# Kernel optimization log

Measured on AMD Instinct MI355X. Metric: run time of the kernel, lower is better.

Reference implementation:

```python
import jax, jax.numpy as jnp
import numpy as np

B, N, DIN, DOUT, DA = 8, 2048, 128, 128, 2
NEG_SLOPE = 0.2


def setup_inputs() -> dict:
    key = jax.random.key(0)
    k = jax.random.split(key, 7)
    x = jax.random.normal(k[0], (B, N, DIN), dtype=jnp.float32)
    mask = jax.random.randint(k[1], (B, N, N), 0, 2, dtype=jnp.int32)
    s = 1.0 / np.sqrt(DIN)
    Wr = jax.random.uniform(k[2], (DA, DIN), jnp.float32, -s, s)      # linear_row.weight
    Wc = jax.random.uniform(k[3], (DA, DIN), jnp.float32, -s, s)      # linear_col.weight
    sa = 1.0 / np.sqrt(2 * DA)
    Wcat = jax.random.uniform(k[4], (2 * DA,), jnp.float32, -sa, sa)  # linear_concat.weight [1, 2*DA] flattened
    Wx = jax.random.uniform(k[5], (DOUT, DIN), jnp.float32, -s, s)    # linear_x.weight
    bx = jax.random.uniform(k[6], (DOUT,), jnp.float32, -s, s)        # linear_x.bias
    return {"x": x, "mask": mask, "Wr": Wr, "Wc": Wc, "Wcat": Wcat, "Wx": Wx, "bx": bx}


def reference(x, mask, Wr, Wc, Wcat, Wx, bx):
    # Row/col projections to tiny attention dim: [B, N, DA]
    row = jnp.einsum('bnd,ad->bna', x, Wr)
    col = jnp.einsum('bnd,ad->bna', x, Wc)
    # Concat scoring: e_ij = linear_concat(LeakyReLU(cat(row_i, col_j)))
    # decomposes as a1 . LR(row_i) + a2 . LR(col_j) -- avoids materializing [B,N,N,2*DA]
    a1, a2 = Wcat[:DA], Wcat[DA:]
    lr_row = jax.nn.leaky_relu(row, NEG_SLOPE) @ a1   # [B, N]
    lr_col = jax.nn.leaky_relu(col, NEG_SLOPE) @ a2   # [B, N]
    e = lr_row[:, :, None] + lr_col[:, None, :]       # [B, N, N]
    # Masked softmax over columns j
    e = jnp.where(mask > 0, e, jnp.float32(-1e9))
    atten = jax.nn.softmax(e, axis=-1)                # [B, N, N]
    # Value projection + combine
    xv = jnp.einsum('bnd,od->bno', x, Wx) + bx        # [B, N, DOUT]
    out = jnp.einsum('bij,bjo->bio', atten, xv)       # [B, N, DOUT]
    return out
```

## Files before the change

### kernel.cpp

```cpp
#include <hip/hip_runtime.h>


typedef __bf16 bf16x8 __attribute__((ext_vector_type(8)));
typedef __bf16 bf16x4 __attribute__((ext_vector_type(4)));
typedef float  f32x4  __attribute__((ext_vector_type(4)));
typedef int    i32x4  __attribute__((ext_vector_type(4)));

#define MFMA_BF16(a, b, c) __builtin_amdgcn_mfma_f32_16x16x32_bf16((a), (b), (c), 0, 0, 0)

static __device__ __forceinline__ bf16x8 cvt8(f32x4 a, f32x4 b) {
  bf16x8 r;
  r[0] = (__bf16)a[0]; r[1] = (__bf16)a[1]; r[2] = (__bf16)a[2]; r[3] = (__bf16)a[3];
  r[4] = (__bf16)b[0]; r[5] = (__bf16)b[1]; r[6] = (__bf16)b[2]; r[7] = (__bf16)b[3];
  return r;
}

__global__ __launch_bounds__(256) void prep_kernel(
    const float* __restrict__ x, const float* __restrict__ Wc,
    const float* __restrict__ Wcat, const float* __restrict__ Wx,
    const float* __restrict__ bx, __bf16* __restrict__ u,
    __bf16* __restrict__ wcol)
{
  __shared__ __bf16 lds[8192];
  const int blk = blockIdx.x;
  const int b = blk >> 5, mt = blk & 31;
  const int wv = threadIdx.x >> 6, lane = threadIdx.x & 63;
  const int np = lane & 15, G = lane >> 4;
  const int r0 = mt * 64 + wv * 16;

  const float* xp = x + ((size_t)(b * 2048 + r0 + np)) * 128 + G * 8;
  bf16x8 af[4];
#pragma unroll
  for (int kk = 0; kk < 4; ++kk) {
    f32x4 x0 = *(const f32x4*)(xp + kk * 32);
    f32x4 x1 = *(const f32x4*)(xp + kk * 32 + 4);
    af[kk] = cvt8(x0, x1);
  }

  f32x4 acc[8], accC;
#pragma unroll
  for (int n = 0; n < 8; ++n) { acc[n][0] = 0.f; acc[n][1] = 0.f; acc[n][2] = 0.f; acc[n][3] = 0.f; }
  accC[0] = accC[1] = accC[2] = accC[3] = 0.f;

#pragma unroll
  for (int n = 0; n < 8; ++n) {
    const float* wp = Wx + (n * 16 + np) * 128 + G * 8;
#pragma unroll
    for (int kk = 0; kk < 4; ++kk) {
      f32x4 w0 = *(const f32x4*)(wp + kk * 32);
      f32x4 w1 = *(const f32x4*)(wp + kk * 32 + 4);
      acc[n] = MFMA_BF16(af[kk], cvt8(w0, w1), acc[n]);
    }
  }
#pragma unroll
  for (int kk = 0; kk < 4; ++kk) {
    bf16x8 bf;
    if (np < 2) {
      const float* cp = Wc + np * 128 + kk * 32 + G * 8;
      f32x4 c0 = *(const f32x4*)cp;
      f32x4 c1 = *(const f32x4*)(cp + 4);
      bf = cvt8(c0, c1);
    } else {
#pragma unroll
      for (int j = 0; j < 8; ++j) bf[j] = (__bf16)0.0f;
    }
    accC = MFMA_BF16(af[kk], bf, accC);
  }

  const float a20 = Wcat[2], a21 = Wcat[3];
  float wexp[4];
#pragma unroll
  for (int r = 0; r < 4; ++r) {
    float c0 = __shfl(accC[r], lane & 48);
    float c1 = __shfl(accC[r], (lane & 48) | 1);
    c0 = c0 > 0.f ? c0 : 0.2f * c0;
    c1 = c1 > 0.f ? c1 : 0.2f * c1;
    wexp[r] = __expf(c0 * a20 + c1 * a21);
  }
  if (np == 0) {
    bf16x4 w4;
#pragma unroll
    for (int r = 0; r < 4; ++r) w4[r] = (__bf16)wexp[r];
    *(bf16x4*)(wcol + (size_t)b * 2048 + r0 + 4 * G) = w4;
  }

  const int t_rel = wv >> 1;
  const int g_store = (wv & 1) * 2 + (G >> 1);
  const int j0 = (G & 1) * 4;
#pragma unroll
  for (int n = 0; n < 8; ++n) {
    float bxv = bx[n * 16 + np];
    bf16x4 v;
#pragma unroll
    for (int r = 0; r < 4; ++r) v[r] = (__bf16)(wexp[r] * (acc[n][r] + bxv));
    *(bf16x4*)(&lds[(t_rel * 8 + n) * 512 + g_store * 128 + np * 8 + j0]) = v;
  }
  __syncthreads();
  __bf16* dst = u + ((size_t)(b * 64 + mt * 2)) * 4096;
#pragma unroll
  for (int it = 0; it < 4; ++it) {
    int s = it * 256 + threadIdx.x;
    ((i32x4*)dst)[s] = ((const i32x4*)lds)[s];
  }
}

__global__ __launch_bounds__(256) void attn_kernel(
    const int* __restrict__ mask, const __bf16* __restrict__ u,
    const __bf16* __restrict__ wcol, float* __restrict__ out)
{
  const int b = blockIdx.x & 7, mt = blockIdx.x >> 3;
  const int wv = threadIdx.x >> 6, lane = threadIdx.x & 63;
  const int np = lane & 15, G = lane >> 4;
  const int row0 = mt * 64 + wv * 16;
  const long long N = 2048;

  const int* mp = mask + ((size_t)b * N + row0 + np) * N + G * 8;
  const __bf16* up = u + (size_t)b * 64 * 4096 + lane * 8;
  const __bf16* wp = wcol + (size_t)b * 2048 + G * 8;

  f32x4 acc[9];
#pragma unroll
  for (int n = 0; n < 9; ++n) { acc[n][0] = 0.f; acc[n][1] = 0.f; acc[n][2] = 0.f; acc[n][3] = 0.f; }

  i32x4 m0A, m1A, m0B, m1B;
  bf16x8 ufA[8], ufB[8], wfA, wfB;

#define LOADS(t, m0, m1, uf, wf)                                         \
  do {                                                                   \
    const int* mpt = mp + (t) * 32;                                      \
    m0 = *(const i32x4*)mpt;                                             \
    m1 = *(const i32x4*)(mpt + 4);                                       \
    const __bf16* upt = up + (t) * 4096;                                 \
    _Pragma("unroll")                                                    \
    for (int n = 0; n < 8; ++n) uf[n] = *(const bf16x8*)(upt + n * 512); \
    wf = *(const bf16x8*)(wp + (t) * 32);                                \
  } while (0)

#define COMPS(m0, m1, uf, wf)                                            \
  do {                                                                   \
    const __bf16 ONE = (__bf16)1.0f, ZER = (__bf16)0.0f;                 \
    bf16x8 af;                                                           \
    af[0] = m0[0] ? ONE : ZER; af[1] = m0[1] ? ONE : ZER;                \
    af[2] = m0[2] ? ONE : ZER; af[3] = m0[3] ? ONE : ZER;                \
    af[4] = m1[0] ? ONE : ZER; af[5] = m1[1] ? ONE : ZER;                \
    af[6] = m1[2] ? ONE : ZER; af[7] = m1[3] ? ONE : ZER;                \
    bf16x8 wfrag;                                                        \
    _Pragma("unroll")                                                    \
    for (int j = 0; j < 8; ++j) wfrag[j] = (np == 0) ? wf[j] : ZER;      \
    _Pragma("unroll")                                                    \
    for (int n = 0; n < 8; ++n) acc[n] = MFMA_BF16(af, uf[n], acc[n]);   \
    acc[8] = MFMA_BF16(af, wfrag, acc[8]);                               \
  } while (0)

  LOADS(0, m0A, m1A, ufA, wfA);
  LOADS(1, m0B, m1B, ufB, wfB);
  for (int t = 0; t < 64; t += 2) {
    COMPS(m0A, m1A, ufA, wfA);
    if (t + 2 < 64) LOADS(t + 2, m0A, m1A, ufA, wfA);
    COMPS(m0B, m1B, ufB, wfB);
    if (t + 3 < 64) LOADS(t + 3, m0B, m1B, ufB, wfB);
  }
#undef LOADS
#undef COMPS

#pragma unroll
  for (int r = 0; r < 4; ++r) {
    float den = __shfl(acc[8][r], lane & 48);
    float inv = 1.0f / den;
    float* op = out + ((size_t)b * N + row0 + 4 * G + r) * 128 + np;
#pragma unroll
    for (int n = 0; n < 8; ++n) op[n * 16] = acc[n][r] * inv;
  }
}

extern "C" void kernel_launch(void* const* d_in, const int* in_sizes, int n_in,
                              void* d_out, int out_size, void* d_ws, size_t ws_size,
                              hipStream_t stream) {
  const float* x    = (const float*)d_in[0];
  const int*   mask = (const int*)d_in[1];
  const float* Wc   = (const float*)d_in[3];
  const float* Wcat = (const float*)d_in[4];
  const float* Wx   = (const float*)d_in[5];
  const float* bx   = (const float*)d_in[6];
  float* out = (float*)d_out;

  const size_t U_BYTES = (size_t)8 * 64 * 4096 * 2;
  if (ws_size < U_BYTES + 8 * 2048 * 2) return;
  __bf16* u    = (__bf16*)d_ws;
  __bf16* wcol = (__bf16*)((char*)d_ws + U_BYTES);

  prep_kernel<<<256, 256, 0, stream>>>(x, Wc, Wcat, Wx, bx, u, wcol);
  attn_kernel<<<256, 256, 0, stream>>>(mask, u, wcol, out);
}
```

Baseline: 237.9 us.

## Split attention K-dimension across waves with LDS reduction, quadruple grid size

Each attention block now handles 16 rows instead of 64, and its four waves split the 2048-column reduction into four quarters, combining partial accumulators through shared memory. The grid grows from 256 to 1024 blocks and launch bounds request 4 blocks per CU, so more waves can be in flight to hide the latency of the mask stream. The cost is a 36 KB LDS reduction, an extra barrier, and every block re-reading its own slice of u and wcol.

```diff
diff --git a/kernel.cpp b/kernel.cpp
--- a/kernel.cpp
+++ b/kernel.cpp
@@ -104,19 +104,19 @@
   }
 }
 
-__global__ __launch_bounds__(256) void attn_kernel(
+__global__ __launch_bounds__(256, 4) void attn_kernel(
     const int* __restrict__ mask, const __bf16* __restrict__ u,
     const __bf16* __restrict__ wcol, float* __restrict__ out)
 {
-  const int b = blockIdx.x & 7, mt = blockIdx.x >> 3;
+  const int b = blockIdx.x & 7, rt = blockIdx.x >> 3;
   const int wv = threadIdx.x >> 6, lane = threadIdx.x & 63;
   const int np = lane & 15, G = lane >> 4;
-  const int row0 = mt * 64 + wv * 16;
+  const int row0 = rt * 16;
   const long long N = 2048;
 
-  const int* mp = mask + ((size_t)b * N + row0 + np) * N + G * 8;
-  const __bf16* up = u + (size_t)b * 64 * 4096 + lane * 8;
-  const __bf16* wp = wcol + (size_t)b * 2048 + G * 8;
+  const int* mp = mask + ((size_t)b * N + row0 + np) * N + wv * 512 + G * 8;
+  const __bf16* up = u + (size_t)b * 64 * 4096 + (size_t)wv * 16 * 4096 + lane * 8;
+  const __bf16* wp = wcol + (size_t)b * 2048 + wv * 512 + G * 8;
 
   f32x4 acc[9];
 #pragma unroll
@@ -154,22 +154,38 @@
 
   LOADS(0, m0A, m1A, ufA, wfA);
   LOADS(1, m0B, m1B, ufB, wfB);
-  for (int t = 0; t < 64; t += 2) {
+  for (int t = 0; t < 16; t += 2) {
     COMPS(m0A, m1A, ufA, wfA);
-    if (t + 2 < 64) LOADS(t + 2, m0A, m1A, ufA, wfA);
+    if (t + 2 < 16) LOADS(t + 2, m0A, m1A, ufA, wfA);
     COMPS(m0B, m1B, ufB, wfB);
-    if (t + 3 < 64) LOADS(t + 3, m0B, m1B, ufB, wfB);
+    if (t + 3 < 16) LOADS(t + 3, m0B, m1B, ufB, wfB);
   }
 #undef LOADS
 #undef COMPS
 
+  __shared__ f32x4 red[36 * 64];
+#pragma unroll
+  for (int n = 0; n < 9; ++n) red[(n * 4 + wv) * 64 + lane] = acc[n];
+  __syncthreads();
+
+  const int n0 = wv * 2, n1 = wv * 2 + 1;
+  f32x4 den4 = red[(8 * 4 + 0) * 64 + lane];
+  f32x4 a0   = red[(n0 * 4 + 0) * 64 + lane];
+  f32x4 a1   = red[(n1 * 4 + 0) * 64 + lane];
+#pragma unroll
+  for (int w = 1; w < 4; ++w) {
+    den4 += red[(8 * 4 + w) * 64 + lane];
+    a0   += red[(n0 * 4 + w) * 64 + lane];
+    a1   += red[(n1 * 4 + w) * 64 + lane];
+  }
+
 #pragma unroll
   for (int r = 0; r < 4; ++r) {
-    float den = __shfl(acc[8][r], lane & 48);
+    float den = __shfl(den4[r], lane & 48);
     float inv = 1.0f / den;
     float* op = out + ((size_t)b * N + row0 + 4 * G + r) * 128 + np;
-#pragma unroll
-    for (int n = 0; n < 8; ++n) op[n * 16] = acc[n][r] * inv;
+    op[n0 * 16] = a0[r] * inv;
+    op[n1 * 16] = a1[r] * inv;
   }
 }
 
@@ -190,5 +206,5 @@
   __bf16* wcol = (__bf16*)((char*)d_ws + U_BYTES);
 
   prep_kernel<<<256, 256, 0, stream>>>(x, Wc, Wcat, Wx, bx, u, wcol);
-  attn_kernel<<<256, 256, 0, stream>>>(mask, u, wcol, out);
-}
+  attn_kernel<<<1024, 256, 0, stream>>>(mask, u, wcol, out);
+}
```

After: 285.3 us. 1.2x slower.

## Split attention work across output columns and deepen mask prefetch pipeline

Applied to the files above, without the earlier changes.

Each block now handles 16 rows instead of 64, and its four waves divide the 128 output columns (two 16-column tiles each) instead of each wave owning separate rows. The grid grows from 256 to 1024 blocks to fill more CUs and raise occupancy through fewer accumulator registers. Mask loads are prefetched four tiles ahead, while u loads stay two ahead. The four waves in a block read the same mask rows, so the gain relies on L2/cache hits, and the denominator MFMA is now computed redundantly in every wave.

```diff
diff --git a/kernel.cpp b/kernel.cpp
--- a/kernel.cpp
+++ b/kernel.cpp
@@ -108,68 +108,80 @@
     const int* __restrict__ mask, const __bf16* __restrict__ u,
     const __bf16* __restrict__ wcol, float* __restrict__ out)
 {
-  const int b = blockIdx.x & 7, mt = blockIdx.x >> 3;
+  const int b = blockIdx.x & 7, rt = blockIdx.x >> 3;
   const int wv = threadIdx.x >> 6, lane = threadIdx.x & 63;
   const int np = lane & 15, G = lane >> 4;
-  const int row0 = mt * 64 + wv * 16;
+  const int row0 = rt * 16;
   const long long N = 2048;
+  const int n0 = wv * 2, n1 = n0 + 1;
 
   const int* mp = mask + ((size_t)b * N + row0 + np) * N + G * 8;
   const __bf16* up = u + (size_t)b * 64 * 4096 + lane * 8;
   const __bf16* wp = wcol + (size_t)b * 2048 + G * 8;
 
-  f32x4 acc[9];
-#pragma unroll
-  for (int n = 0; n < 9; ++n) { acc[n][0] = 0.f; acc[n][1] = 0.f; acc[n][2] = 0.f; acc[n][3] = 0.f; }
-
-  i32x4 m0A, m1A, m0B, m1B;
-  bf16x8 ufA[8], ufB[8], wfA, wfB;
-
-#define LOADS(t, m0, m1, uf, wf)                                         \
-  do {                                                                   \
-    const int* mpt = mp + (t) * 32;                                      \
-    m0 = *(const i32x4*)mpt;                                             \
-    m1 = *(const i32x4*)(mpt + 4);                                       \
-    const __bf16* upt = up + (t) * 4096;                                 \
-    _Pragma("unroll")                                                    \
-    for (int n = 0; n < 8; ++n) uf[n] = *(const bf16x8*)(upt + n * 512); \
-    wf = *(const bf16x8*)(wp + (t) * 32);                                \
+  f32x4 accN0, accN1, accD;
+  accN0[0]=accN0[1]=accN0[2]=accN0[3]=0.f;
+  accN1[0]=accN1[1]=accN1[2]=accN1[3]=0.f;
+  accD[0]=accD[1]=accD[2]=accD[3]=0.f;
+
+  i32x4 M0_0, M1_0, M0_1, M1_1, M0_2, M1_2, M0_3, M1_3;
+  bf16x8 u0A, u1A, wA, u0B, u1B, wB;
+
+#define LOADM(s, t)                                   \
+  do {                                                \
+    const int* p = mp + (t) * 32;                     \
+    M0_##s = *(const i32x4*)p;                        \
+    M1_##s = *(const i32x4*)(p + 4);                  \
   } while (0)
 
-#define COMPS(m0, m1, uf, wf)                                            \
+#define LOADU(buf, t)                                 \
+  do {                                                \
+    const __bf16* p = up + (size_t)(t) * 4096;        \
+    u0##buf = *(const bf16x8*)(p + n0 * 512);         \
+    u1##buf = *(const bf16x8*)(p + n1 * 512);         \
+    w##buf = *(const bf16x8*)(wp + (t) * 32);         \
+  } while (0)
+
+#define COMP(s, buf)                                                     \
   do {                                                                   \
     const __bf16 ONE = (__bf16)1.0f, ZER = (__bf16)0.0f;                 \
     bf16x8 af;                                                           \
-    af[0] = m0[0] ? ONE : ZER; af[1] = m0[1] ? ONE : ZER;                \
-    af[2] = m0[2] ? ONE : ZER; af[3] = m0[3] ? ONE : ZER;                \
-    af[4] = m1[0] ? ONE : ZER; af[5] = m1[1] ? ONE : ZER;                \
-    af[6] = m1[2] ? ONE : ZER; af[7] = m1[3] ? ONE : ZER;                \
+    af[0] = M0_##s[0] ? ONE : ZER; af[1] = M0_##s[1] ? ONE : ZER;        \
+    af[2] = M0_##s[2] ? ONE : ZER; af[3] = M0_##s[3] ? ONE : ZER;        \
+    af[4] = M1_##s[0] ? ONE : ZER; af[5] = M1_##s[1] ? ONE : ZER;        \
+    af[6] = M1_##s[2] ? ONE : ZER; af[7] = M1_##s[3] ? ONE : ZER;        \
     bf16x8 wfrag;                                                        \
     _Pragma("unroll")                                                    \
-    for (int j = 0; j < 8; ++j) wfrag[j] = (np == 0) ? wf[j] : ZER;      \
-    _Pragma("unroll")                                                    \
-    for (int n = 0; n < 8; ++n) acc[n] = MFMA_BF16(af, uf[n], acc[n]);   \
-    acc[8] = MFMA_BF16(af, wfrag, acc[8]);                               \
+    for (int j = 0; j < 8; ++j) wfrag[j] = (np == 0) ? w##buf[j] : ZER;  \
+    accN0 = MFMA_BF16(af, u0##buf, accN0);                               \
+    accN1 = MFMA_BF16(af, u1##buf, accN1);                               \
+    accD  = MFMA_BF16(af, wfrag, accD);                                  \
   } while (0)
 
-  LOADS(0, m0A, m1A, ufA, wfA);
-  LOADS(1, m0B, m1B, ufB, wfB);
-  for (int t = 0; t < 64; t += 2) {
-    COMPS(m0A, m1A, ufA, wfA);
-    if (t + 2 < 64) LOADS(t + 2, m0A, m1A, ufA, wfA);
-    COMPS(m0B, m1B, ufB, wfB);
-    if (t + 3 < 64) LOADS(t + 3, m0B, m1B, ufB, wfB);
-  }
-#undef LOADS
-#undef COMPS
+  LOADM(0, 0); LOADM(1, 1); LOADM(2, 2); LOADM(3, 3);
+  LOADU(A, 0); LOADU(B, 1);
+
+  for (int t = 0; t < 60; t += 4) {
+    COMP(0, A); LOADM(0, t + 4); LOADU(A, t + 2);
+    COMP(1, B); LOADM(1, t + 5); LOADU(B, t + 3);
+    COMP(2, A); LOADM(2, t + 6); LOADU(A, t + 4);
+    COMP(3, B); LOADM(3, t + 7); LOADU(B, t + 5);
+  }
+  COMP(0, A); LOADU(A, 62);
+  COMP(1, B); LOADU(B, 63);
+  COMP(2, A);
+  COMP(3, B);
+#undef LOADM
+#undef LOADU
+#undef COMP
 
 #pragma unroll
   for (int r = 0; r < 4; ++r) {
-    float den = __shfl(acc[8][r], lane & 48);
+    float den = __shfl(accD[r], lane & 48);
     float inv = 1.0f / den;
     float* op = out + ((size_t)b * N + row0 + 4 * G + r) * 128 + np;
-#pragma unroll
-    for (int n = 0; n < 8; ++n) op[n * 16] = acc[n][r] * inv;
+    op[n0 * 16] = accN0[r] * inv;
+    op[n1 * 16] = accN1[r] * inv;
   }
 }
 
@@ -190,5 +202,5 @@
   __bf16* wcol = (__bf16*)((char*)d_ws + U_BYTES);
 
   prep_kernel<<<256, 256, 0, stream>>>(x, Wc, Wcat, Wx, bx, u, wcol);
-  attn_kernel<<<256, 256, 0, stream>>>(mask, u, wcol, out);
-}
+  attn_kernel<<<1024, 256, 0, stream>>>(mask, u, wcol, out);
+}
```

Measured after the change: 291.5 us. 1.23x slower.

## Stage mask tiles into LDS via async global_load_lds and split output columns across waves

Applied to the files above, without the earlier changes.

The attention kernel now streams mask tiles for 32 rows into double-buffered, XOR-swizzled shared memory with direct global-to-LDS loads. Each wave handles two output column blocks plus the denominator column instead of all eight, and the grid doubles to 512 blocks. The exp(col) weights are folded into the u buffer as a ninth padded column block, which removes the separate wcol array and the per-lane zero masking. This is meant to raise occupancy and overlap mask streaming with MFMA work, at the cost of LDS usage, block-wide barriers and more redundant u reads per block.

```diff
diff --git a/kernel.cpp b/kernel.cpp
--- a/kernel.cpp
+++ b/kernel.cpp
@@ -5,8 +5,14 @@
 typedef __bf16 bf16x4 __attribute__((ext_vector_type(4)));
 typedef float  f32x4  __attribute__((ext_vector_type(4)));
 typedef int    i32x4  __attribute__((ext_vector_type(4)));
+typedef unsigned int u32;
 
 #define MFMA_BF16(a, b, c) __builtin_amdgcn_mfma_f32_16x16x32_bf16((a), (b), (c), 0, 0, 0)
+
+#define GLOAD_LDS16(gp, lp)                                                     \
+  __builtin_amdgcn_global_load_lds(                                             \
+      (const __attribute__((address_space(1))) void*)(gp),                      \
+      (__attribute__((address_space(3))) void*)(lp), 16, 0, 0)
 
 static __device__ __forceinline__ bf16x8 cvt8(f32x4 a, f32x4 b) {
   bf16x8 r;
@@ -18,10 +24,9 @@
 __global__ __launch_bounds__(256) void prep_kernel(
     const float* __restrict__ x, const float* __restrict__ Wc,
     const float* __restrict__ Wcat, const float* __restrict__ Wx,
-    const float* __restrict__ bx, __bf16* __restrict__ u,
-    __bf16* __restrict__ wcol)
+    const float* __restrict__ bx, __bf16* __restrict__ u)
 {
-  __shared__ __bf16 lds[8192];
+  __shared__ __bf16 lds[9216];
   const int blk = blockIdx.x;
   const int b = blk >> 5, mt = blk & 31;
   const int wv = threadIdx.x >> 6, lane = threadIdx.x & 63;
@@ -77,12 +82,6 @@
     c1 = c1 > 0.f ? c1 : 0.2f * c1;
     wexp[r] = __expf(c0 * a20 + c1 * a21);
   }
-  if (np == 0) {
-    bf16x4 w4;
-#pragma unroll
-    for (int r = 0; r < 4; ++r) w4[r] = (__bf16)wexp[r];
-    *(bf16x4*)(wcol + (size_t)b * 2048 + r0 + 4 * G) = w4;
-  }
 
   const int t_rel = wv >> 1;
   const int g_store = (wv & 1) * 2 + (G >> 1);
@@ -93,83 +92,97 @@
     bf16x4 v;
 #pragma unroll
     for (int r = 0; r < 4; ++r) v[r] = (__bf16)(wexp[r] * (acc[n][r] + bxv));
-    *(bf16x4*)(&lds[(t_rel * 8 + n) * 512 + g_store * 128 + np * 8 + j0]) = v;
+    *(bf16x4*)(&lds[(t_rel * 9 + n) * 512 + g_store * 128 + np * 8 + j0]) = v;
+  }
+  {
+    bf16x4 v8;
+#pragma unroll
+    for (int r = 0; r < 4; ++r) v8[r] = (np == 0) ? (__bf16)wexp[r] : (__bf16)0.0f;
+    *(bf16x4*)(&lds[(t_rel * 9 + 8) * 512 + g_store * 128 + np * 8 + j0]) = v8;
   }
   __syncthreads();
-  __bf16* dst = u + ((size_t)(b * 64 + mt * 2)) * 4096;
-#pragma unroll
-  for (int it = 0; it < 4; ++it) {
-    int s = it * 256 + threadIdx.x;
+  __bf16* dst = u + ((size_t)(b * 64 + mt * 2)) * 9 * 512;
+  for (int s = threadIdx.x; s < 1152; s += 256)
     ((i32x4*)dst)[s] = ((const i32x4*)lds)[s];
-  }
 }
 
 __global__ __launch_bounds__(256) void attn_kernel(
     const int* __restrict__ mask, const __bf16* __restrict__ u,
-    const __bf16* __restrict__ wcol, float* __restrict__ out)
+    float* __restrict__ out)
 {
-  const int b = blockIdx.x & 7, mt = blockIdx.x >> 3;
+  __shared__ int smask[2 * 4096];
+  const int b = blockIdx.x & 7, rt = blockIdx.x >> 3;
   const int wv = threadIdx.x >> 6, lane = threadIdx.x & 63;
   const int np = lane & 15, G = lane >> 4;
-  const int row0 = mt * 64 + wv * 16;
-  const long long N = 2048;
-
-  const int* mp = mask + ((size_t)b * N + row0 + np) * N + G * 8;
-  const __bf16* up = u + (size_t)b * 64 * 4096 + lane * 8;
-  const __bf16* wp = wcol + (size_t)b * 2048 + G * 8;
-
-  f32x4 acc[9];
-#pragma unroll
-  for (int n = 0; n < 9; ++n) { acc[n][0] = 0.f; acc[n][1] = 0.f; acc[n][2] = 0.f; acc[n][3] = 0.f; }
-
-  i32x4 m0A, m1A, m0B, m1B;
-  bf16x8 ufA[8], ufB[8], wfA, wfB;
-
-#define LOADS(t, m0, m1, uf, wf)                                         \
-  do {                                                                   \
-    const int* mpt = mp + (t) * 32;                                      \
-    m0 = *(const i32x4*)mpt;                                             \
-    m1 = *(const i32x4*)(mpt + 4);                                       \
-    const __bf16* upt = up + (t) * 4096;                                 \
-    _Pragma("unroll")                                                    \
-    for (int n = 0; n < 8; ++n) uf[n] = *(const bf16x8*)(upt + n * 512); \
-    wf = *(const bf16x8*)(wp + (t) * 32);                                \
+  const int row0 = rt * 32;
+  const int n0 = wv * 2, n1 = n0 + 1;
+  const int swz = (np & 7) << 2;
+  const int hl = lane >> 5, cb = (lane & 31) * 16;
+
+  const char* gbase = (const char*)(mask + ((size_t)b * 2048 + row0) * 2048);
+  const __bf16* up = u + (size_t)b * 64 * 9 * 512 + lane * 8;
+
+  f32x4 acc[2][3];
+#pragma unroll
+  for (int mi = 0; mi < 2; ++mi)
+#pragma unroll
+    for (int n = 0; n < 3; ++n) { acc[mi][n][0] = 0.f; acc[mi][n][1] = 0.f; acc[mi][n][2] = 0.f; acc[mi][n][3] = 0.f; }
+
+#define STAGE(it, nb)                                                          \
+  do {                                                                         \
+    char* lbase = (char*)smask + (nb) * 16384 + wv * 4096;                     \
+    _Pragma("unroll")                                                          \
+    for (int i = 0; i < 4; ++i) {                                              \
+      int lr = wv * 8 + i * 2 + hl;                                            \
+      const char* gp = gbase + (size_t)lr * 8192 + (it) * 512 +                \
+                       (cb ^ (((i * 2 + hl) & 7) << 4));                       \
+      GLOAD_LDS16(gp, lbase + i * 1024);                                       \
+    }                                                                          \
   } while (0)
 
-#define COMPS(m0, m1, uf, wf)                                            \
-  do {                                                                   \
-    const __bf16 ONE = (__bf16)1.0f, ZER = (__bf16)0.0f;                 \
-    bf16x8 af;                                                           \
-    af[0] = m0[0] ? ONE : ZER; af[1] = m0[1] ? ONE : ZER;                \
-    af[2] = m0[2] ? ONE : ZER; af[3] = m0[3] ? ONE : ZER;                \
-    af[4] = m1[0] ? ONE : ZER; af[5] = m1[1] ? ONE : ZER;                \
-    af[6] = m1[2] ? ONE : ZER; af[7] = m1[3] ? ONE : ZER;                \
-    bf16x8 wfrag;                                                        \
-    _Pragma("unroll")                                                    \
-    for (int j = 0; j < 8; ++j) wfrag[j] = (np == 0) ? wf[j] : ZER;      \
-    _Pragma("unroll")                                                    \
-    for (int n = 0; n < 8; ++n) acc[n] = MFMA_BF16(af, uf[n], acc[n]);   \
-    acc[8] = MFMA_BF16(af, wfrag, acc[8]);                               \
-  } while (0)
-
-  LOADS(0, m0A, m1A, ufA, wfA);
-  LOADS(1, m0B, m1B, ufB, wfB);
-  for (int t = 0; t < 64; t += 2) {
-    COMPS(m0A, m1A, ufA, wfA);
-    if (t + 2 < 64) LOADS(t + 2, m0A, m1A, ufA, wfA);
-    COMPS(m0B, m1B, ufB, wfB);
-    if (t + 3 < 64) LOADS(t + 3, m0B, m1B, ufB, wfB);
-  }
-#undef LOADS
-#undef COMPS
-
-#pragma unroll
-  for (int r = 0; r < 4; ++r) {
-    float den = __shfl(acc[8][r], lane & 48);
-    float inv = 1.0f / den;
-    float* op = out + ((size_t)b * N + row0 + 4 * G + r) * 128 + np;
-#pragma unroll
-    for (int n = 0; n < 8; ++n) op[n * 16] = acc[n][r] * inv;
+  STAGE(0, 0);
+  __syncthreads();
+
+  for (int it = 0; it < 16; ++it) {
+    if (it < 15) STAGE(it + 1, (it + 1) & 1);
+    const u32* cur = (const u32*)smask + (it & 1) * 4096;
+#pragma unroll
+    for (int tk = 0; tk < 4; ++tk) {
+      const int t = it * 4 + tk;
+      const __bf16* ut = up + (size_t)(t * 9) * 512;
+      bf16x8 U0 = *(const bf16x8*)(ut + n0 * 512);
+      bf16x8 U1 = *(const bf16x8*)(ut + n1 * 512);
+      bf16x8 UD = *(const bf16x8*)(ut + 8 * 512);
+      const int X = tk * 32 + G * 8;
+#pragma unroll
+      for (int mi = 0; mi < 2; ++mi) {
+        const u32* rp = cur + (mi * 16 + np) * 128;
+        i32x4 ma = *(const i32x4*)(rp + (X ^ swz));
+        i32x4 mb = *(const i32x4*)(rp + ((X + 4) ^ swz));
+        union { u32 w[4]; bf16x8 v; } A;
+        A.w[0] = (ma[0] ? 0x3F80u : 0u) | (ma[1] ? 0x3F800000u : 0u);
+        A.w[1] = (ma[2] ? 0x3F80u : 0u) | (ma[3] ? 0x3F800000u : 0u);
+        A.w[2] = (mb[0] ? 0x3F80u : 0u) | (mb[1] ? 0x3F800000u : 0u);
+        A.w[3] = (mb[2] ? 0x3F80u : 0u) | (mb[3] ? 0x3F800000u : 0u);
+        acc[mi][0] = MFMA_BF16(A.v, U0, acc[mi][0]);
+        acc[mi][1] = MFMA_BF16(A.v, U1, acc[mi][1]);
+        acc[mi][2] = MFMA_BF16(A.v, UD, acc[mi][2]);
+      }
+    }
+    __syncthreads();
+  }
+#undef STAGE
+
+#pragma unroll
+  for (int mi = 0; mi < 2; ++mi) {
+#pragma unroll
+    for (int r = 0; r < 4; ++r) {
+      float den = __shfl(acc[mi][2][r], lane & 48);
+      float inv = 1.0f / den;
+      float* op = out + ((size_t)b * 2048 + row0 + mi * 16 + 4 * G + r) * 128 + np;
+      op[n0 * 16] = acc[mi][0][r] * inv;
+      op[n1 * 16] = acc[mi][1][r] * inv;
+    }
   }
 }
 
@@ -184,11 +197,10 @@
   const float* bx   = (const float*)d_in[6];
   float* out = (float*)d_out;
 
-  const size_t U_BYTES = (size_t)8 * 64 * 4096 * 2;
-  if (ws_size < U_BYTES + 8 * 2048 * 2) return;
-  __bf16* u    = (__bf16*)d_ws;
-  __bf16* wcol = (__bf16*)((char*)d_ws + U_BYTES);
-
-  prep_kernel<<<256, 256, 0, stream>>>(x, Wc, Wcat, Wx, bx, u, wcol);
-  attn_kernel<<<256, 256, 0, stream>>>(mask, u, wcol, out);
-}
+  const size_t U_BYTES = (size_t)8 * 64 * 9 * 512 * 2;
+  if (ws_size < U_BYTES) return;
+  __bf16* u = (__bf16*)d_ws;
+
+  prep_kernel<<<256, 256, 0, stream>>>(x, Wc, Wcat, Wx, bx, u);
+  attn_kernel<<<512, 256, 0, stream>>>(mask, u, out);
+}
```

Result: faster. 227.5 us (-4.4%).
